# Kernel tuning notes

Hardware: AMD Instinct MI355X
Metric: run time of the kernel (lower is better)

## Reference

```python
import jax, jax.numpy as jnp
import numpy as np

B, Q, D, H, W_OUT = 1024, 128, 64, 256, 32
PI = float(np.pi)
LN_EPS = 1e-5


def setup_inputs() -> dict:
    key = jax.random.key(0)
    ks = jax.random.split(key, 18)

    def u(k, shape, fan_in):
        s = 1.0 / np.sqrt(fan_in)
        return jax.random.uniform(k, shape, jnp.float32, -s, s)

    return {
        "x_in": jax.random.normal(ks[0], (B, Q, D), jnp.float32),
        "w_out": W_OUT,
        # fc_feat: Linear(3D -> H)
        "Wf": u(ks[1], (H, 3 * D), 3 * D), "bf": u(ks[2], (H,), 3 * D),
        # GRUCell(H, H): torch layout W_ih[3H,H], W_hh[3H,H]
        "W_ih": u(ks[3], (3 * H, H), H), "W_hh": u(ks[4], (3 * H, H), H),
        "b_ih": u(ks[5], (3 * H,), H), "b_hh": u(ks[6], (3 * H,), H),
        # LayerNorm(H)
        "ln_g": jnp.ones((H,), jnp.float32), "ln_b": jnp.zeros((H,), jnp.float32),
        # fc_gain: Linear(H -> D)
        "Wg": u(ks[7], (D, H), H), "bg": u(ks[8], (D,), H),
        # fc_rp: Linear(H -> 2)
        "Wrp": u(ks[9], (2, H), H), "brp": u(ks[10], (2,), H),
        # roll_gru: GRUCell(H+D, H)
        "W_ih_r": u(ks[11], (3 * H, H + D), H), "W_hh_r": u(ks[12], (3 * H, H), H),
        "b_ih_r": u(ks[13], (3 * H,), H), "b_hh_r": u(ks[14], (3 * H,), H),
        # fc_rp_r: Linear(H -> 2)
        "Wrpr": u(ks[15], (2, H), H), "brpr": u(ks[16], (2,), H),
    }


def _gru_cell(x, h, W_ih, W_hh, b_ih, b_hh):
    gi = x @ W_ih.T + b_ih      # [B,3H]
    gh = h @ W_hh.T + b_hh      # [B,3H]
    i_r, i_z, i_n = jnp.split(gi, 3, axis=-1)
    h_r, h_z, h_n = jnp.split(gh, 3, axis=-1)
    r = jax.nn.sigmoid(i_r + h_r)
    z = jax.nn.sigmoid(i_z + h_z)
    n = jnp.tanh(i_n + r * h_n)
    return (1.0 - z) * n + z * h


def _layernorm(x, g, b):
    mu = jnp.mean(x, axis=-1, keepdims=True)
    var = jnp.mean(jnp.square(x - mu), axis=-1, keepdims=True)
    return (x - mu) * jax.lax.rsqrt(var + LN_EPS) * g + b


def _rotate(x, rho, phi):
    M = x.shape[-1] // 2
    re, im = x[:, :M], x[:, M:]
    c, s = jnp.cos(phi), jnp.sin(phi)
    return jnp.concatenate([rho * (c * re - s * im), rho * (s * re + c * im)], axis=1)


def _forward(x_in, w_out, Wf, bf, W_ih, W_hh, b_ih, b_hh, ln_g, ln_b,
             Wg, bg, Wrp, brp, W_ih_r, W_hh_r, b_ih_r, b_hh_r, Wrpr, brpr):
    Bsz, q, Dd = x_in.shape
    y0 = x_in[:, 0, :]
    h0 = jnp.zeros((Bsz, W_ih.shape[1]), x_in.dtype)
    upd0 = jnp.zeros((Bsz, Dd), x_in.dtype)

    def enc_step(carry, y_t):
        x_post, h, y_prev, prev_upd = carry
        feat = jnp.concatenate([y_t - y_prev, y_t - x_post, prev_upd], axis=1)
        zf = jnp.tanh(feat @ Wf.T + bf)
        h = _layernorm(_gru_cell(zf, h, W_ih, W_hh, b_ih, b_hh), ln_g, ln_b)
        rp = h @ Wrp.T + brp
        rho = jax.nn.sigmoid(rp[:, 0:1]) * 1.25
        phi = PI * jnp.tanh(rp[:, 1:2])
        x_pri = _rotate(x_post, rho, phi)
        K = jax.nn.sigmoid(h @ Wg.T + bg)
        x_post_new = x_pri + K * (y_t - x_pri)
        return (x_post_new, h, y_t, x_post_new - x_pri), None

    ys = jnp.swapaxes(x_in, 0, 1)  # [q,B,D]
    (x_post, h, _, _), _ = jax.lax.scan(enc_step, (y0, h0, y0, upd0), ys)

    def roll_step(carry, _):
        h_r, curr = carry
        h_r = _layernorm(_gru_cell(jnp.concatenate([h_r, curr], axis=1), h_r,
                                   W_ih_r, W_hh_r, b_ih_r, b_hh_r), ln_g, ln_b)
        rp = h_r @ Wrpr.T + brpr
        rho = jax.nn.sigmoid(rp[:, 0:1]) * 1.25
        phi = PI * jnp.tanh(rp[:, 1:2])
        curr = _rotate(curr, rho, phi)
        return (h_r, curr), curr

    _, preds = jax.lax.scan(roll_step, (h, x_post), None, length=w_out)  # [w_out,B,D]
    return jnp.swapaxes(preds, 0, 1)  # [B,w_out,D]


def reference(x_in, w_out, Wf, bf, W_ih, W_hh, b_ih, b_hh, ln_g, ln_b,
              Wg, bg, Wrp, brp, W_ih_r, W_hh_r, b_ih_r, b_hh_r, Wrpr, brpr):
    return _forward(x_in, w_out, Wf, bf, W_ih, W_hh, b_ih, b_hh, ln_g, ln_b,
                    Wg, bg, Wrp, brp, W_ih_r, W_hh_r, b_ih_r, b_hh_r, Wrpr, brpr)
```

## Files before the change

kernel.cpp:

```cpp
#include <hip/hip_runtime.h>

#define QLEN 128
#define WOUT 32
#define ROWS 4
#define PI_F 3.14159265358979f

typedef __attribute__((ext_vector_type(2))) float f32x2;

#define OFF_BF    0
#define OFF_BIH   256
#define OFF_BHH   1024
#define OFF_LNG   1792
#define OFF_LNB   2048
#define OFF_BG    2304
#define OFF_BRP   2368
#define OFF_BIHR  2370
#define OFF_BHHR  3138
#define OFF_BRPR  3906
#define OFF_WRP   3908
#define OFF_WRPR  4420
#define SB_TOTAL  4932

__device__ __forceinline__ float sigm(float x){ return 1.0f/(1.0f + __expf(-x)); }
__device__ __forceinline__ float tanh_f(float x){ return 2.0f/(1.0f + __expf(-2.0f*x)) - 1.0f; }

__device__ __forceinline__ void barrier_lgkm(){
  asm volatile("s_waitcnt lgkmcnt(0)" ::: "memory");
  __builtin_amdgcn_s_barrier();
  asm volatile("" ::: "memory");
}

__device__ __forceinline__ void pkfma(f32x2& acc, f32x2 a, f32x2 b){
  asm("v_pk_fma_f32 %0, %1, %2, %0" : "+v"(acc) : "v"(a), "v"(b));
}
__device__ __forceinline__ void fma4p(f32x2& acc, const float4& a, const float4& w){
  f32x2 alo = {a.x, a.y}, ahi = {a.z, a.w};
  f32x2 wlo = {w.x, w.y}, whi = {w.z, w.w};
  pkfma(acc, alo, wlo); pkfma(acc, ahi, whi);
}
__device__ __forceinline__ float hadd(f32x2 v){ return v[0] + v[1]; }

__global__ void transpose_w(const float* __restrict__ src, float* __restrict__ dst, int N, int K){
  int i = blockIdx.x*blockDim.x + threadIdx.x;
  if (i < N*K){
    int c = i / K; int k = i - c*K;
    dst[(size_t)(((k>>2)*N + c)<<2) + (k&3)] = src[i];
  }
}

__global__ __launch_bounds__(1024) void knet_v9(
  const float* __restrict__ x_in,
  const float* __restrict__ t_wf,
  const float* __restrict__ t_wih,
  const float* __restrict__ t_whh,
  const float* __restrict__ t_wg,
  const float* __restrict__ t_wihr,
  const float* __restrict__ t_whhr,
  const float* __restrict__ p_bf,  const float* __restrict__ p_bih, const float* __restrict__ p_bhh,
  const float* __restrict__ p_lng, const float* __restrict__ p_lnb,
  const float* __restrict__ p_bg,  const float* __restrict__ p_wrp, const float* __restrict__ p_brp,
  const float* __restrict__ p_bihr,const float* __restrict__ p_bhhr,
  const float* __restrict__ p_wrpr,const float* __restrict__ p_brpr,
  float* __restrict__ out)
{
  __shared__ __align__(16) float sb[SB_TOTAL];
  __shared__ __align__(16) float s_h  [ROWS][260];
  __shared__ __align__(16) float s_pre[ROWS][260];
  __shared__ __align__(16) float s_zf [ROWS][260];
  __shared__ __align__(16) float s_feat[ROWS][196];
  __shared__ __align__(16) float s_x  [ROWS][64];
  __shared__ __align__(16) float s_part[4][6][ROWS][256];
  __shared__ float s_rho[ROWS], s_phi[ROWS];

  const int tid = threadIdx.x;
  const int gb0 = blockIdx.x * ROWS;

  if (tid<256){ sb[OFF_BF+tid]=p_bf[tid]; sb[OFF_LNG+tid]=p_lng[tid]; sb[OFF_LNB+tid]=p_lnb[tid]; }
  if (tid<768){ sb[OFF_BIH+tid]=p_bih[tid]; sb[OFF_BHH+tid]=p_bhh[tid]; sb[OFF_BIHR+tid]=p_bihr[tid]; sb[OFF_BHHR+tid]=p_bhhr[tid]; }
  if (tid<64)  sb[OFF_BG+tid]=p_bg[tid];
  if (tid<512){ sb[OFF_WRP+tid]=p_wrp[tid]; sb[OFF_WRPR+tid]=p_wrpr[tid]; }
  if (tid<2){ sb[OFF_BRP+tid]=p_brp[tid]; sb[OFF_BRPR+tid]=p_brpr[tid]; }
  for (int e=tid; e<ROWS*256; e+=1024){ s_h[e>>8][e&255]=0.f; }

  const int w    = tid >> 6;
  const int lane = tid & 63;
  const int g4   = tid >> 8;
  const int j256 = tid & 255;
  const int j6   = tid & 63;

  const int pr = tid >> 6;
  const int pd = tid & 63;
  float y_cur = 0.f, x_st = 0.f;
  if (tid < 256){
    y_cur = x_in[(size_t)(gb0+pr)*(QLEN*64) + pd];
    x_st  = y_cur;
    s_x[pr][pd] = x_st;
    s_feat[pr][pd] = 0.f; s_feat[pr][64+pd] = 0.f; s_feat[pr][128+pd] = 0.f;
  }

  const float4* tf  = (const float4*)t_wf;
  const float4* tih = (const float4*)t_wih;
  const float4* thh = (const float4*)t_whh;
  const float4* tg  = (const float4*)t_wg;
  const float4* tir = (const float4*)t_wihr;
  const float4* th2 = (const float4*)t_whhr;
  const int k0B = g4*12;
  const int k0C = g4*16;

  __syncthreads();

  auto ln_rp = [&](int wrpO, int brpO){
    if (w < ROWS){
      const int row = w;
      const int c0  = lane << 2;
      float4 v = *(const float4*)&s_pre[row][c0];
      float sum = v.x+v.y+v.z+v.w;
      float ss  = v.x*v.x + v.y*v.y + v.z*v.z + v.w*v.w;
      #pragma unroll
      for (int m=1;m<64;m<<=1){ sum += __shfl_xor(sum,m); ss += __shfl_xor(ss,m); }
      float mu = sum * (1.f/256.f);
      float rs = rsqrtf(ss*(1.f/256.f) - mu*mu + 1e-5f);
      float4 hn;
      hn.x = (v.x-mu)*rs*sb[OFF_LNG+c0  ] + sb[OFF_LNB+c0  ];
      hn.y = (v.y-mu)*rs*sb[OFF_LNG+c0+1] + sb[OFF_LNB+c0+1];
      hn.z = (v.z-mu)*rs*sb[OFF_LNG+c0+2] + sb[OFF_LNB+c0+2];
      hn.w = (v.w-mu)*rs*sb[OFF_LNG+c0+3] + sb[OFF_LNB+c0+3];
      *(float4*)&s_h[row][c0] = hn;
      float p0 = hn.x*sb[wrpO+c0] + hn.y*sb[wrpO+c0+1] + hn.z*sb[wrpO+c0+2] + hn.w*sb[wrpO+c0+3];
      float p1 = hn.x*sb[wrpO+256+c0] + hn.y*sb[wrpO+256+c0+1] + hn.z*sb[wrpO+256+c0+2] + hn.w*sb[wrpO+256+c0+3];
      #pragma unroll
      for (int m=1;m<64;m<<=1){ p0 += __shfl_xor(p0,m); p1 += __shfl_xor(p1,m); }
      if (lane==0){
        s_rho[row] = 1.25f * sigm(p0 + sb[brpO]);
        s_phi[row] = PI_F * tanh_f(p1 + sb[brpO+1]);
      }
    }
  };

  #pragma unroll 1
  for (int t=0; t<QLEN; ++t){
    float y_next = 0.f;
    if (tid < 256){
      const int tn = (t+1<QLEN)? t+1 : QLEN-1;
      y_next = x_in[(size_t)(gb0+pr)*(QLEN*64) + (size_t)tn*64 + pd];
    }

    {
      f32x2 a0={0.f,0.f},a1={0.f,0.f},a2={0.f,0.f},a3={0.f,0.f};
      #pragma unroll 4
      for (int k4=k0B;k4<k0B+12;k4++){
        float4 wv = tf[k4*256 + j256];
        float4 f0=*(const float4*)&s_feat[0][k4<<2];
        float4 f1=*(const float4*)&s_feat[1][k4<<2];
        float4 f2=*(const float4*)&s_feat[2][k4<<2];
        float4 f3=*(const float4*)&s_feat[3][k4<<2];
        fma4p(a0,f0,wv); fma4p(a1,f1,wv); fma4p(a2,f2,wv); fma4p(a3,f3,wv);
      }
      s_part[g4][0][0][j256]=hadd(a0); s_part[g4][0][1][j256]=hadd(a1);
      s_part[g4][0][2][j256]=hadd(a2); s_part[g4][0][3][j256]=hadd(a3);
    }
    {
      f32x2 a[3][ROWS];
      #pragma unroll
      for (int gg=0;gg<3;gg++)
        #pragma unroll
        for (int ri=0;ri<ROWS;ri++) a[gg][ri]=(f32x2){0.f,0.f};
      #pragma unroll 2
      for (int k4=k0C;k4<k0C+16;k4++){
        const int base=k4*768 + j256;
        float4 whr=thh[base], whz=thh[base+256], whn=thh[base+512];
        #pragma unroll
        for (int ri=0;ri<ROWS;ri++){
          float4 ah=*(const float4*)&s_h[ri][k4<<2];
          fma4p(a[0][ri],ah,whr); fma4p(a[1][ri],ah,whz); fma4p(a[2][ri],ah,whn);
        }
      }
      #pragma unroll
      for (int gg=0;gg<3;gg++)
        #pragma unroll
        for (int ri=0;ri<ROWS;ri++)
          s_part[g4][3+gg][ri][j256]=hadd(a[gg][ri]);
    }
    barrier_lgkm();

    {
      const int r=tid>>8, jj=tid&255;
      s_zf[r][jj] = tanh_f(s_part[0][0][r][jj]+s_part[1][0][r][jj]
                          +s_part[2][0][r][jj]+s_part[3][0][r][jj] + sb[OFF_BF+jj]);
    }
    barrier_lgkm();

    {
      f32x2 a[3][ROWS];
      #pragma unroll
      for (int gg=0;gg<3;gg++)
        #pragma unroll
        for (int ri=0;ri<ROWS;ri++) a[gg][ri]=(f32x2){0.f,0.f};
      #pragma unroll 4
      for (int k4=k0C;k4<k0C+16;k4++){
        const int base=k4*768 + j256;
        float4 wir=tih[base], wiz=tih[base+256], win=tih[base+512];
        #pragma unroll
        for (int ri=0;ri<ROWS;ri++){
          float4 az=*(const float4*)&s_zf[ri][k4<<2];
          fma4p(a[0][ri],az,wir); fma4p(a[1][ri],az,wiz); fma4p(a[2][ri],az,win);
        }
      }
      #pragma unroll
      for (int gg=0;gg<3;gg++)
        #pragma unroll
        for (int ri=0;ri<ROWS;ri++)
          s_part[g4][gg][ri][j256]=hadd(a[gg][ri]);
    }
    barrier_lgkm();

    {
      const int r=tid>>8, jj=tid&255;
      float s0=s_part[0][0][r][jj]+s_part[1][0][r][jj]+s_part[2][0][r][jj]+s_part[3][0][r][jj];
      float s1=s_part[0][1][r][jj]+s_part[1][1][r][jj]+s_part[2][1][r][jj]+s_part[3][1][r][jj];
      float s2=s_part[0][2][r][jj]+s_part[1][2][r][jj]+s_part[2][2][r][jj]+s_part[3][2][r][jj];
      float s3=s_part[0][3][r][jj]+s_part[1][3][r][jj]+s_part[2][3][r][jj]+s_part[3][3][r][jj];
      float s4=s_part[0][4][r][jj]+s_part[1][4][r][jj]+s_part[2][4][r][jj]+s_part[3][4][r][jj];
      float s5=s_part[0][5][r][jj]+s_part[1][5][r][jj]+s_part[2][5][r][jj]+s_part[3][5][r][jj];
      float r_ = sigm(s0+sb[OFF_BIH+jj]     + s3+sb[OFF_BHH+jj]);
      float z_ = sigm(s1+sb[OFF_BIH+256+jj] + s4+sb[OFF_BHH+256+jj]);
      float n_ = tanh_f(s2+sb[OFF_BIH+512+jj] + r_*(s5+sb[OFF_BHH+512+jj]));
      s_pre[r][jj] = (1.f - z_)*n_ + z_*s_h[r][jj];
    }
    barrier_lgkm();

    ln_rp(OFF_WRP, OFF_BRP);
    barrier_lgkm();

    {
      f32x2 acc[ROWS];
      #pragma unroll
      for (int ri=0;ri<ROWS;ri++) acc[ri]=(f32x2){0.f,0.f};
      const int kb = w*4;
      #pragma unroll
      for (int q=0;q<4;q++){
        float4 wv = tg[(kb+q)*64 + j6];
        #pragma unroll
        for (int ri=0;ri<ROWS;ri++){
          float4 ah=*(const float4*)&s_h[ri][(kb+q)<<2];
          fma4p(acc[ri],ah,wv);
        }
      }
      #pragma unroll
      for (int ri=0;ri<ROWS;ri++) s_part[w>>2][0][ri][(w&3)*64 + j6] = hadd(acc[ri]);
    }
    barrier_lgkm();

    if (tid < 256){
      float kacc = sb[OFF_BG+pd];
      #pragma unroll
      for (int q=0;q<16;q++) kacc += s_part[q>>2][0][pr][(q&3)*64+pd];
      float kg = sigm(kacc);
      float rho=s_rho[pr], phi=s_phi[pr];
      float sn,cs; __sincosf(phi,&sn,&cs);
      float px = __shfl_xor(x_st,32);
      float pre = (pd<32) ? rho*(cs*x_st - sn*px) : rho*(sn*px + cs*x_st);
      float del = kg*(y_cur - pre);
      x_st = pre + del;
      s_x[pr][pd] = x_st;
      s_feat[pr][pd]      = y_next - y_cur;
      s_feat[pr][64+pd]   = y_next - x_st;
      s_feat[pr][128+pd]  = del;
      y_cur = y_next;
    }
    barrier_lgkm();
  }

  #pragma unroll 1
  for (int u=0; u<WOUT; ++u){
    {
      f32x2 a[6][ROWS];
      #pragma unroll
      for (int gg=0;gg<6;gg++)
        #pragma unroll
        for (int ri=0;ri<ROWS;ri++) a[gg][ri]=(f32x2){0.f,0.f};
      if (g4 < 3){
        const int k0i=g4*20;
        #pragma unroll 2
        for (int k4=k0i;k4<k0i+20;k4++){
          const int base=k4*768 + j256;
          float4 wir=tir[base], wiz=tir[base+256], win=tir[base+512];
          #pragma unroll
          for (int ri=0;ri<ROWS;ri++){
            float4 ah=*(const float4*)&s_h[ri][k4<<2];
            fma4p(a[0][ri],ah,wir); fma4p(a[1][ri],ah,wiz); fma4p(a[2][ri],ah,win);
          }
        }
      } else {
        #pragma unroll
        for (int k4=60;k4<64;k4++){
          const int base=k4*768 + j256;
          float4 wir=tir[base], wiz=tir[base+256], win=tir[base+512];
          #pragma unroll
          for (int ri=0;ri<ROWS;ri++){
            float4 ah=*(const float4*)&s_h[ri][k4<<2];
            fma4p(a[0][ri],ah,wir); fma4p(a[1][ri],ah,wiz); fma4p(a[2][ri],ah,win);
          }
        }
        #pragma unroll 2
        for (int k4=64;k4<80;k4++){
          const int base=k4*768 + j256;
          float4 wir=tir[base], wiz=tir[base+256], win=tir[base+512];
          #pragma unroll
          for (int ri=0;ri<ROWS;ri++){
            float4 ax=*(const float4*)&s_x[ri][(k4-64)<<2];
            fma4p(a[0][ri],ax,wir); fma4p(a[1][ri],ax,wiz); fma4p(a[2][ri],ax,win);
          }
        }
      }
      {
        #pragma unroll 2
        for (int k4=k0C;k4<k0C+16;k4++){
          const int base=k4*768 + j256;
          float4 whr=th2[base], whz=th2[base+256], whn=th2[base+512];
          #pragma unroll
          for (int ri=0;ri<ROWS;ri++){
            float4 ah=*(const float4*)&s_h[ri][k4<<2];
            fma4p(a[3][ri],ah,whr); fma4p(a[4][ri],ah,whz); fma4p(a[5][ri],ah,whn);
          }
        }
      }
      #pragma unroll
      for (int gg=0;gg<6;gg++)
        #pragma unroll
        for (int ri=0;ri<ROWS;ri++)
          s_part[g4][gg][ri][j256]=hadd(a[gg][ri]);
    }
    barrier_lgkm();

    {
      const int r=tid>>8, jj=tid&255;
      float s0=s_part[0][0][r][jj]+s_part[1][0][r][jj]+s_part[2][0][r][jj]+s_part[3][0][r][jj];
      float s1=s_part[0][1][r][jj]+s_part[1][1][r][jj]+s_part[2][1][r][jj]+s_part[3][1][r][jj];
      float s2=s_part[0][2][r][jj]+s_part[1][2][r][jj]+s_part[2][2][r][jj]+s_part[3][2][r][jj];
      float s3=s_part[0][3][r][jj]+s_part[1][3][r][jj]+s_part[2][3][r][jj]+s_part[3][3][r][jj];
      float s4=s_part[0][4][r][jj]+s_part[1][4][r][jj]+s_part[2][4][r][jj]+s_part[3][4][r][jj];
      float s5=s_part[0][5][r][jj]+s_part[1][5][r][jj]+s_part[2][5][r][jj]+s_part[3][5][r][jj];
      float r_ = sigm(s0+sb[OFF_BIHR+jj]     + s3+sb[OFF_BHHR+jj]);
      float z_ = sigm(s1+sb[OFF_BIHR+256+jj] + s4+sb[OFF_BHHR+256+jj]);
      float n_ = tanh_f(s2+sb[OFF_BIHR+512+jj] + r_*(s5+sb[OFF_BHHR+512+jj]));
      s_pre[r][jj] = (1.f - z_)*n_ + z_*s_h[r][jj];
    }
    barrier_lgkm();

    ln_rp(OFF_WRPR, OFF_BRPR);
    barrier_lgkm();

    if (tid < 256){
      float rho=s_rho[pr], phi=s_phi[pr];
      float sn,cs; __sincosf(phi,&sn,&cs);
      float px = __shfl_xor(x_st,32);
      float nx = (pd<32) ? rho*(cs*x_st - sn*px) : rho*(sn*px + cs*x_st);
      x_st = nx;
      s_x[pr][pd] = nx;
      out[(size_t)(gb0+pr)*(WOUT*64) + (size_t)u*64 + pd] = nx;
    }
    barrier_lgkm();
  }
}

extern "C" void kernel_launch(void* const* d_in, const int* in_sizes, int n_in,
                              void* d_out, int out_size, void* d_ws, size_t ws_size,
                              hipStream_t stream){
  const float* x_in = (const float*)d_in[0];
  const float* Wf   = (const float*)d_in[2];
  const float* bf_  = (const float*)d_in[3];
  const float* Wih  = (const float*)d_in[4];
  const float* Whh  = (const float*)d_in[5];
  const float* bih  = (const float*)d_in[6];
  const float* bhh  = (const float*)d_in[7];
  const float* lng  = (const float*)d_in[8];
  const float* lnb  = (const float*)d_in[9];
  const float* Wg   = (const float*)d_in[10];
  const float* bg   = (const float*)d_in[11];
  const float* Wrp  = (const float*)d_in[12];
  const float* brp  = (const float*)d_in[13];
  const float* Wihr = (const float*)d_in[14];
  const float* Whhr = (const float*)d_in[15];
  const float* bihr = (const float*)d_in[16];
  const float* bhhr = (const float*)d_in[17];
  const float* Wrpr = (const float*)d_in[18];
  const float* brpr = (const float*)d_in[19];

  float* ws = (float*)d_ws;
  float* t_wf   = ws;
  float* t_wih  = ws + 49152;
  float* t_whh  = ws + 245760;
  float* t_wg   = ws + 442368;
  float* t_wihr = ws + 458752;
  float* t_whhr = ws + 704512;

  transpose_w<<<(49152 +255)/256, 256, 0, stream>>>(Wf,   t_wf,   256, 192);
  transpose_w<<<(196608+255)/256, 256, 0, stream>>>(Wih,  t_wih,  768, 256);
  transpose_w<<<(196608+255)/256, 256, 0, stream>>>(Whh,  t_whh,  768, 256);
  transpose_w<<<(16384 +255)/256, 256, 0, stream>>>(Wg,   t_wg,   64,  256);
  transpose_w<<<(245760+255)/256, 256, 0, stream>>>(Wihr, t_wihr, 768, 320);
  transpose_w<<<(196608+255)/256, 256, 0, stream>>>(Whhr, t_whhr, 768, 256);

  knet_v9<<<256, 1024, 0, stream>>>(x_in, t_wf, t_wih, t_whh, t_wg, t_wihr, t_whhr,
      bf_, bih, bhh, lng, lnb, bg, Wrp, brp, bihr, bhhr, Wrpr, brpr,
      (float*)d_out);
}
```

Baseline: 2.986 ms.

## Fold LayerNorm into gain matmul and prefetch first weight tiles across barriers

Precomputes Wg scaled by the LayerNorm gain together with per-output constants, so the Kalman gain is computed from the pre-norm hidden state with a mean/rstd correction. This lets waves 4-5 run the gain matmul concurrently with the LN/rp wave, which removes one barrier per encoder step. It also prefetches the first k-slice of the Wf, Whh, Wih and Wih_r weights before barriers to hide global-load latency, at the cost of extra live registers. Folding the LayerNorm changes rounding slightly.

```diff
diff --git a/kernel.cpp b/kernel.cpp
--- a/kernel.cpp
+++ b/kernel.cpp
@@ -19,7 +19,9 @@
 #define OFF_BRPR  3906
 #define OFF_WRP   3908
 #define OFF_WRPR  4420
-#define SB_TOTAL  4932
+#define OFF_C1    4932
+#define OFF_C2    4996
+#define SB_TOTAL  5060
 
 __device__ __forceinline__ float sigm(float x){ return 1.0f/(1.0f + __expf(-x)); }
 __device__ __forceinline__ float tanh_f(float x){ return 2.0f/(1.0f + __expf(-2.0f*x)) - 1.0f; }
@@ -48,17 +50,35 @@
   }
 }
 
-__global__ __launch_bounds__(1024) void knet_v9(
+__global__ void prep_wg(const float* __restrict__ Wg, const float* __restrict__ lng,
+                        const float* __restrict__ lnb, const float* __restrict__ bg,
+                        float* __restrict__ wg2, float* __restrict__ c1, float* __restrict__ c2){
+  int j = threadIdx.x;
+  if (j < 64){
+    float a1=0.f, a2=0.f;
+    for (int k=0;k<256;k++){
+      float wv = Wg[j*256+k];
+      float gw = lng[k]*wv;
+      wg2[(size_t)(((k>>2)*64 + j)<<2) + (k&3)] = gw;
+      a1 += gw;
+      a2 += lnb[k]*wv;
+    }
+    c1[j]=a1; c2[j]=a2+bg[j];
+  }
+}
+
+__global__ __launch_bounds__(1024) void knet_v10(
   const float* __restrict__ x_in,
   const float* __restrict__ t_wf,
   const float* __restrict__ t_wih,
   const float* __restrict__ t_whh,
-  const float* __restrict__ t_wg,
+  const float* __restrict__ wg2p,
   const float* __restrict__ t_wihr,
   const float* __restrict__ t_whhr,
+  const float* __restrict__ c1p, const float* __restrict__ c2p,
   const float* __restrict__ p_bf,  const float* __restrict__ p_bih, const float* __restrict__ p_bhh,
   const float* __restrict__ p_lng, const float* __restrict__ p_lnb,
-  const float* __restrict__ p_bg,  const float* __restrict__ p_wrp, const float* __restrict__ p_brp,
+  const float* __restrict__ p_wrp, const float* __restrict__ p_brp,
   const float* __restrict__ p_bihr,const float* __restrict__ p_bhhr,
   const float* __restrict__ p_wrpr,const float* __restrict__ p_brpr,
   float* __restrict__ out)
@@ -70,14 +90,14 @@
   __shared__ __align__(16) float s_feat[ROWS][196];
   __shared__ __align__(16) float s_x  [ROWS][64];
   __shared__ __align__(16) float s_part[4][6][ROWS][256];
-  __shared__ float s_rho[ROWS], s_phi[ROWS];
+  __shared__ float s_rho[ROWS], s_phi[ROWS], s_mu[ROWS], s_rs[ROWS];
 
   const int tid = threadIdx.x;
   const int gb0 = blockIdx.x * ROWS;
 
   if (tid<256){ sb[OFF_BF+tid]=p_bf[tid]; sb[OFF_LNG+tid]=p_lng[tid]; sb[OFF_LNB+tid]=p_lnb[tid]; }
   if (tid<768){ sb[OFF_BIH+tid]=p_bih[tid]; sb[OFF_BHH+tid]=p_bhh[tid]; sb[OFF_BIHR+tid]=p_bihr[tid]; sb[OFF_BHHR+tid]=p_bhhr[tid]; }
-  if (tid<64)  sb[OFF_BG+tid]=p_bg[tid];
+  if (tid<64){ sb[OFF_C1+tid]=c1p[tid]; sb[OFF_C2+tid]=c2p[tid]; }
   if (tid<512){ sb[OFF_WRP+tid]=p_wrp[tid]; sb[OFF_WRPR+tid]=p_wrpr[tid]; }
   if (tid<2){ sb[OFF_BRP+tid]=p_brp[tid]; sb[OFF_BRPR+tid]=p_brpr[tid]; }
   for (int e=tid; e<ROWS*256; e+=1024){ s_h[e>>8][e&255]=0.f; }
@@ -86,7 +106,6 @@
   const int lane = tid & 63;
   const int g4   = tid >> 8;
   const int j256 = tid & 255;
-  const int j6   = tid & 63;
 
   const int pr = tid >> 6;
   const int pd = tid & 63;
@@ -101,7 +120,7 @@
   const float4* tf  = (const float4*)t_wf;
   const float4* tih = (const float4*)t_wih;
   const float4* thh = (const float4*)t_whh;
-  const float4* tg  = (const float4*)t_wg;
+  const float4* tg2 = (const float4*)wg2p;
   const float4* tir = (const float4*)t_wihr;
   const float4* th2 = (const float4*)t_whhr;
   const int k0B = g4*12;
@@ -133,9 +152,16 @@
       if (lane==0){
         s_rho[row] = 1.25f * sigm(p0 + sb[brpO]);
         s_phi[row] = PI_F * tanh_f(p1 + sb[brpO+1]);
+        s_mu[row] = mu; s_rs[row] = rs;
       }
     }
   };
+
+  float4 pfA, pfB0, pfB1, pfB2;
+  pfA  = tf [(size_t)k0B*256 + j256];
+  pfB0 = thh[(size_t)k0C*768 + j256];
+  pfB1 = thh[(size_t)k0C*768 + 256 + j256];
+  pfB2 = thh[(size_t)k0C*768 + 512 + j256];
 
   #pragma unroll 1
   for (int t=0; t<QLEN; ++t){
@@ -147,8 +173,15 @@
 
     {
       f32x2 a0={0.f,0.f},a1={0.f,0.f},a2={0.f,0.f},a3={0.f,0.f};
+      {
+        float4 f0=*(const float4*)&s_feat[0][k0B<<2];
+        float4 f1=*(const float4*)&s_feat[1][k0B<<2];
+        float4 f2=*(const float4*)&s_feat[2][k0B<<2];
+        float4 f3=*(const float4*)&s_feat[3][k0B<<2];
+        fma4p(a0,f0,pfA); fma4p(a1,f1,pfA); fma4p(a2,f2,pfA); fma4p(a3,f3,pfA);
+      }
       #pragma unroll 4
-      for (int k4=k0B;k4<k0B+12;k4++){
+      for (int k4=k0B+1;k4<k0B+12;k4++){
         float4 wv = tf[k4*256 + j256];
         float4 f0=*(const float4*)&s_feat[0][k4<<2];
         float4 f1=*(const float4*)&s_feat[1][k4<<2];
@@ -165,8 +198,13 @@
       for (int gg=0;gg<3;gg++)
         #pragma unroll
         for (int ri=0;ri<ROWS;ri++) a[gg][ri]=(f32x2){0.f,0.f};
-      #pragma unroll 2
-      for (int k4=k0C;k4<k0C+16;k4++){
+      #pragma unroll
+      for (int ri=0;ri<ROWS;ri++){
+        float4 ah=*(const float4*)&s_h[ri][k0C<<2];
+        fma4p(a[0][ri],ah,pfB0); fma4p(a[1][ri],ah,pfB1); fma4p(a[2][ri],ah,pfB2);
+      }
+      #pragma unroll 4
+      for (int k4=k0C+1;k4<k0C+16;k4++){
         const int base=k4*768 + j256;
         float4 whr=thh[base], whz=thh[base+256], whn=thh[base+512];
         #pragma unroll
@@ -183,6 +221,9 @@
     }
     barrier_lgkm();
 
+    float4 pz0 = tih[(size_t)k0C*768 + j256];
+    float4 pz1 = tih[(size_t)k0C*768 + 256 + j256];
+    float4 pz2 = tih[(size_t)k0C*768 + 512 + j256];
     {
       const int r=tid>>8, jj=tid&255;
       s_zf[r][jj] = tanh_f(s_part[0][0][r][jj]+s_part[1][0][r][jj]
@@ -196,8 +237,13 @@
       for (int gg=0;gg<3;gg++)
         #pragma unroll
         for (int ri=0;ri<ROWS;ri++) a[gg][ri]=(f32x2){0.f,0.f};
+      #pragma unroll
+      for (int ri=0;ri<ROWS;ri++){
+        float4 az=*(const float4*)&s_zf[ri][k0C<<2];
+        fma4p(a[0][ri],az,pz0); fma4p(a[1][ri],az,pz1); fma4p(a[2][ri],az,pz2);
+      }
       #pragma unroll 4
-      for (int k4=k0C;k4<k0C+16;k4++){
+      for (int k4=k0C+1;k4<k0C+16;k4++){
         const int base=k4*768 + j256;
         float4 wir=tih[base], wiz=tih[base+256], win=tih[base+512];
         #pragma unroll
@@ -230,32 +276,32 @@
     barrier_lgkm();
 
     ln_rp(OFF_WRP, OFF_BRP);
-    barrier_lgkm();
-
-    {
+    if (w==4 || w==5){
+      const int eg = w-4, ej = lane;
       f32x2 acc[ROWS];
       #pragma unroll
       for (int ri=0;ri<ROWS;ri++) acc[ri]=(f32x2){0.f,0.f};
-      const int kb = w*4;
-      #pragma unroll
-      for (int q=0;q<4;q++){
-        float4 wv = tg[(kb+q)*64 + j6];
+      #pragma unroll 4
+      for (int k4=eg*32; k4<eg*32+32; k4++){
+        float4 wv = tg2[k4*64 + ej];
         #pragma unroll
         for (int ri=0;ri<ROWS;ri++){
-          float4 ah=*(const float4*)&s_h[ri][(kb+q)<<2];
-          fma4p(acc[ri],ah,wv);
-        }
-      }
-      #pragma unroll
-      for (int ri=0;ri<ROWS;ri++) s_part[w>>2][0][ri][(w&3)*64 + j6] = hadd(acc[ri]);
-    }
-    barrier_lgkm();
-
+          float4 ap=*(const float4*)&s_pre[ri][k4<<2];
+          fma4p(acc[ri],ap,wv);
+        }
+      }
+      #pragma unroll
+      for (int ri=0;ri<ROWS;ri++) s_part[eg][0][ri][ej] = hadd(acc[ri]);
+    }
+    barrier_lgkm();
+
+    pfA  = tf [(size_t)k0B*256 + j256];
+    pfB0 = thh[(size_t)k0C*768 + j256];
+    pfB1 = thh[(size_t)k0C*768 + 256 + j256];
+    pfB2 = thh[(size_t)k0C*768 + 512 + j256];
     if (tid < 256){
-      float kacc = sb[OFF_BG+pd];
-      #pragma unroll
-      for (int q=0;q<16;q++) kacc += s_part[q>>2][0][pr][(q&3)*64+pd];
-      float kg = sigm(kacc);
+      float S1 = s_part[0][0][pr][pd] + s_part[1][0][pr][pd];
+      float kg = sigm( s_rs[pr]*(S1 - s_mu[pr]*sb[OFF_C1+pd]) + sb[OFF_C2+pd] );
       float rho=s_rho[pr], phi=s_phi[pr];
       float sn,cs; __sincosf(phi,&sn,&cs);
       float px = __shfl_xor(x_st,32);
@@ -271,6 +317,11 @@
     barrier_lgkm();
   }
 
+  const int k0i = (g4<3)? g4*20 : 60;
+  float4 pi0 = tir[(size_t)k0i*768 + j256];
+  float4 pi1 = tir[(size_t)k0i*768 + 256 + j256];
+  float4 pi2 = tir[(size_t)k0i*768 + 512 + j256];
+
   #pragma unroll 1
   for (int u=0; u<WOUT; ++u){
     {
@@ -279,10 +330,14 @@
       for (int gg=0;gg<6;gg++)
         #pragma unroll
         for (int ri=0;ri<ROWS;ri++) a[gg][ri]=(f32x2){0.f,0.f};
+      #pragma unroll
+      for (int ri=0;ri<ROWS;ri++){
+        float4 ah=*(const float4*)&s_h[ri][k0i<<2];
+        fma4p(a[0][ri],ah,pi0); fma4p(a[1][ri],ah,pi1); fma4p(a[2][ri],ah,pi2);
+      }
       if (g4 < 3){
-        const int k0i=g4*20;
         #pragma unroll 2
-        for (int k4=k0i;k4<k0i+20;k4++){
+        for (int k4=k0i+1;k4<k0i+20;k4++){
           const int base=k4*768 + j256;
           float4 wir=tir[base], wiz=tir[base+256], win=tir[base+512];
           #pragma unroll
@@ -293,7 +348,7 @@
         }
       } else {
         #pragma unroll
-        for (int k4=60;k4<64;k4++){
+        for (int k4=61;k4<64;k4++){
           const int base=k4*768 + j256;
           float4 wir=tir[base], wiz=tir[base+256], win=tir[base+512];
           #pragma unroll
@@ -351,6 +406,9 @@
     ln_rp(OFF_WRPR, OFF_BRPR);
     barrier_lgkm();
 
+    pi0 = tir[(size_t)k0i*768 + j256];
+    pi1 = tir[(size_t)k0i*768 + 256 + j256];
+    pi2 = tir[(size_t)k0i*768 + 512 + j256];
     if (tid < 256){
       float rho=s_rho[pr], phi=s_phi[pr];
       float sn,cs; __sincosf(phi,&sn,&cs);
@@ -391,18 +449,20 @@
   float* t_wf   = ws;
   float* t_wih  = ws + 49152;
   float* t_whh  = ws + 245760;
-  float* t_wg   = ws + 442368;
+  float* wg2    = ws + 442368;
   float* t_wihr = ws + 458752;
   float* t_whhr = ws + 704512;
+  float* c1     = ws + 901120;
+  float* c2     = ws + 901184;
 
   transpose_w<<<(49152 +255)/256, 256, 0, stream>>>(Wf,   t_wf,   256, 192);
   transpose_w<<<(196608+255)/256, 256, 0, stream>>>(Wih,  t_wih,  768, 256);
   transpose_w<<<(196608+255)/256, 256, 0, stream>>>(Whh,  t_whh,  768, 256);
-  transpose_w<<<(16384 +255)/256, 256, 0, stream>>>(Wg,   t_wg,   64,  256);
   transpose_w<<<(245760+255)/256, 256, 0, stream>>>(Wihr, t_wihr, 768, 320);
   transpose_w<<<(196608+255)/256, 256, 0, stream>>>(Whhr, t_whhr, 768, 256);
-
-  knet_v9<<<256, 1024, 0, stream>>>(x_in, t_wf, t_wih, t_whh, t_wg, t_wihr, t_whhr,
-      bf_, bih, bhh, lng, lnb, bg, Wrp, brp, bihr, bhhr, Wrpr, brpr,
+  prep_wg<<<1, 64, 0, stream>>>(Wg, lng, lnb, bg, wg2, c1, c2);
+
+  knet_v10<<<256, 1024, 0, stream>>>(x_in, t_wf, t_wih, t_whh, wg2, t_wihr, t_whhr,
+      c1, c2, bf_, bih, bhh, lng, lnb, Wrp, brp, bihr, bhhr, Wrpr, brpr,
       (float*)d_out);
 }
```

After: 11.05 ms. +270.2%, slower.

## Process eight batch rows per block with 512 threads and two-way K split

Applied to the files above, without the earlier changes.

Doubles rows per block from 4 to 8 and halves threads to 512, so each weight load from global/L2 is reused across twice as many batch rows. The K dimension is now split two ways instead of four, which halves the partial-sum reduction work. Only 128 blocks launch, fewer than the CU count, so parallelism drops and each thread does twice the FMA work per step.

```diff
diff --git a/kernel.cpp b/kernel.cpp
--- a/kernel.cpp
+++ b/kernel.cpp
@@ -2,7 +2,7 @@
 
 #define QLEN 128
 #define WOUT 32
-#define ROWS 4
+#define ROWS 8
 #define PI_F 3.14159265358979f
 
 typedef __attribute__((ext_vector_type(2))) float f32x2;
@@ -48,7 +48,7 @@
   }
 }
 
-__global__ __launch_bounds__(1024) void knet_v9(
+__global__ __launch_bounds__(512, 2) void knet_v13(
   const float* __restrict__ x_in,
   const float* __restrict__ t_wf,
   const float* __restrict__ t_wih,
@@ -69,29 +69,29 @@
   __shared__ __align__(16) float s_zf [ROWS][260];
   __shared__ __align__(16) float s_feat[ROWS][196];
   __shared__ __align__(16) float s_x  [ROWS][64];
-  __shared__ __align__(16) float s_part[4][6][ROWS][256];
+  __shared__ __align__(16) float s_part[2][6][ROWS][256];
   __shared__ float s_rho[ROWS], s_phi[ROWS];
 
   const int tid = threadIdx.x;
   const int gb0 = blockIdx.x * ROWS;
 
-  if (tid<256){ sb[OFF_BF+tid]=p_bf[tid]; sb[OFF_LNG+tid]=p_lng[tid]; sb[OFF_LNB+tid]=p_lnb[tid]; }
-  if (tid<768){ sb[OFF_BIH+tid]=p_bih[tid]; sb[OFF_BHH+tid]=p_bhh[tid]; sb[OFF_BIHR+tid]=p_bihr[tid]; sb[OFF_BHHR+tid]=p_bhhr[tid]; }
-  if (tid<64)  sb[OFF_BG+tid]=p_bg[tid];
-  if (tid<512){ sb[OFF_WRP+tid]=p_wrp[tid]; sb[OFF_WRPR+tid]=p_wrpr[tid]; }
+  for (int i=tid;i<256;i+=512){ sb[OFF_BF+i]=p_bf[i]; sb[OFF_LNG+i]=p_lng[i]; sb[OFF_LNB+i]=p_lnb[i]; }
+  for (int i=tid;i<768;i+=512){ sb[OFF_BIH+i]=p_bih[i]; sb[OFF_BHH+i]=p_bhh[i]; sb[OFF_BIHR+i]=p_bihr[i]; sb[OFF_BHHR+i]=p_bhhr[i]; }
+  for (int i=tid;i<64;i+=512)  sb[OFF_BG+i]=p_bg[i];
+  for (int i=tid;i<512;i+=512){ sb[OFF_WRP+i]=p_wrp[i]; sb[OFF_WRPR+i]=p_wrpr[i]; }
   if (tid<2){ sb[OFF_BRP+tid]=p_brp[tid]; sb[OFF_BRPR+tid]=p_brpr[tid]; }
-  for (int e=tid; e<ROWS*256; e+=1024){ s_h[e>>8][e&255]=0.f; }
+  for (int e=tid; e<ROWS*256; e+=512){ s_h[e>>8][e&255]=0.f; }
 
   const int w    = tid >> 6;
   const int lane = tid & 63;
-  const int g4   = tid >> 8;
+  const int g2   = tid >> 8;
   const int j256 = tid & 255;
   const int j6   = tid & 63;
 
   const int pr = tid >> 6;
   const int pd = tid & 63;
-  float y_cur = 0.f, x_st = 0.f;
-  if (tid < 256){
+  float y_cur, x_st;
+  {
     y_cur = x_in[(size_t)(gb0+pr)*(QLEN*64) + pd];
     x_st  = y_cur;
     s_x[pr][pd] = x_st;
@@ -104,60 +104,60 @@
   const float4* tg  = (const float4*)t_wg;
   const float4* tir = (const float4*)t_wihr;
   const float4* th2 = (const float4*)t_whhr;
-  const int k0B = g4*12;
-  const int k0C = g4*16;
+  const int k0B = g2*24;
+  const int k0C = g2*32;
 
   __syncthreads();
 
   auto ln_rp = [&](int wrpO, int brpO){
-    if (w < ROWS){
-      const int row = w;
-      const int c0  = lane << 2;
-      float4 v = *(const float4*)&s_pre[row][c0];
-      float sum = v.x+v.y+v.z+v.w;
-      float ss  = v.x*v.x + v.y*v.y + v.z*v.z + v.w*v.w;
-      #pragma unroll
-      for (int m=1;m<64;m<<=1){ sum += __shfl_xor(sum,m); ss += __shfl_xor(ss,m); }
-      float mu = sum * (1.f/256.f);
-      float rs = rsqrtf(ss*(1.f/256.f) - mu*mu + 1e-5f);
-      float4 hn;
-      hn.x = (v.x-mu)*rs*sb[OFF_LNG+c0  ] + sb[OFF_LNB+c0  ];
-      hn.y = (v.y-mu)*rs*sb[OFF_LNG+c0+1] + sb[OFF_LNB+c0+1];
-      hn.z = (v.z-mu)*rs*sb[OFF_LNG+c0+2] + sb[OFF_LNB+c0+2];
-      hn.w = (v.w-mu)*rs*sb[OFF_LNG+c0+3] + sb[OFF_LNB+c0+3];
-      *(float4*)&s_h[row][c0] = hn;
-      float p0 = hn.x*sb[wrpO+c0] + hn.y*sb[wrpO+c0+1] + hn.z*sb[wrpO+c0+2] + hn.w*sb[wrpO+c0+3];
-      float p1 = hn.x*sb[wrpO+256+c0] + hn.y*sb[wrpO+256+c0+1] + hn.z*sb[wrpO+256+c0+2] + hn.w*sb[wrpO+256+c0+3];
-      #pragma unroll
-      for (int m=1;m<64;m<<=1){ p0 += __shfl_xor(p0,m); p1 += __shfl_xor(p1,m); }
-      if (lane==0){
-        s_rho[row] = 1.25f * sigm(p0 + sb[brpO]);
-        s_phi[row] = PI_F * tanh_f(p1 + sb[brpO+1]);
-      }
+    const int row = w;
+    const int c0  = lane << 2;
+    float4 v = *(const float4*)&s_pre[row][c0];
+    float sum = v.x+v.y+v.z+v.w;
+    float ss  = v.x*v.x + v.y*v.y + v.z*v.z + v.w*v.w;
+    #pragma unroll
+    for (int m=1;m<64;m<<=1){ sum += __shfl_xor(sum,m); ss += __shfl_xor(ss,m); }
+    float mu = sum * (1.f/256.f);
+    float rs = rsqrtf(ss*(1.f/256.f) - mu*mu + 1e-5f);
+    float4 hn;
+    hn.x = (v.x-mu)*rs*sb[OFF_LNG+c0  ] + sb[OFF_LNB+c0  ];
+    hn.y = (v.y-mu)*rs*sb[OFF_LNG+c0+1] + sb[OFF_LNB+c0+1];
+    hn.z = (v.z-mu)*rs*sb[OFF_LNG+c0+2] + sb[OFF_LNB+c0+2];
+    hn.w = (v.w-mu)*rs*sb[OFF_LNG+c0+3] + sb[OFF_LNB+c0+3];
+    *(float4*)&s_h[row][c0] = hn;
+    float p0 = hn.x*sb[wrpO+c0] + hn.y*sb[wrpO+c0+1] + hn.z*sb[wrpO+c0+2] + hn.w*sb[wrpO+c0+3];
+    float p1 = hn.x*sb[wrpO+256+c0] + hn.y*sb[wrpO+256+c0+1] + hn.z*sb[wrpO+256+c0+2] + hn.w*sb[wrpO+256+c0+3];
+    #pragma unroll
+    for (int m=1;m<64;m<<=1){ p0 += __shfl_xor(p0,m); p1 += __shfl_xor(p1,m); }
+    if (lane==0){
+      s_rho[row] = 1.25f * sigm(p0 + sb[brpO]);
+      s_phi[row] = PI_F * tanh_f(p1 + sb[brpO+1]);
     }
   };
 
   #pragma unroll 1
   for (int t=0; t<QLEN; ++t){
-    float y_next = 0.f;
-    if (tid < 256){
+    float y_next;
+    {
       const int tn = (t+1<QLEN)? t+1 : QLEN-1;
       y_next = x_in[(size_t)(gb0+pr)*(QLEN*64) + (size_t)tn*64 + pd];
     }
 
     {
-      f32x2 a0={0.f,0.f},a1={0.f,0.f},a2={0.f,0.f},a3={0.f,0.f};
+      f32x2 a[ROWS];
+      #pragma unroll
+      for (int ri=0;ri<ROWS;ri++) a[ri]=(f32x2){0.f,0.f};
       #pragma unroll 4
-      for (int k4=k0B;k4<k0B+12;k4++){
+      for (int k4=k0B;k4<k0B+24;k4++){
         float4 wv = tf[k4*256 + j256];
-        float4 f0=*(const float4*)&s_feat[0][k4<<2];
-        float4 f1=*(const float4*)&s_feat[1][k4<<2];
-        float4 f2=*(const float4*)&s_feat[2][k4<<2];
-        float4 f3=*(const float4*)&s_feat[3][k4<<2];
-        fma4p(a0,f0,wv); fma4p(a1,f1,wv); fma4p(a2,f2,wv); fma4p(a3,f3,wv);
-      }
-      s_part[g4][0][0][j256]=hadd(a0); s_part[g4][0][1][j256]=hadd(a1);
-      s_part[g4][0][2][j256]=hadd(a2); s_part[g4][0][3][j256]=hadd(a3);
+        #pragma unroll
+        for (int ri=0;ri<ROWS;ri++){
+          float4 f=*(const float4*)&s_feat[ri][k4<<2];
+          fma4p(a[ri],f,wv);
+        }
+      }
+      #pragma unroll
+      for (int ri=0;ri<ROWS;ri++) s_part[g2][0][ri][j256]=hadd(a[ri]);
     }
     {
       f32x2 a[3][ROWS];
@@ -166,7 +166,7 @@
         #pragma unroll
         for (int ri=0;ri<ROWS;ri++) a[gg][ri]=(f32x2){0.f,0.f};
       #pragma unroll 2
-      for (int k4=k0C;k4<k0C+16;k4++){
+      for (int k4=k0C;k4<k0C+32;k4++){
         const int base=k4*768 + j256;
         float4 whr=thh[base], whz=thh[base+256], whn=thh[base+512];
         #pragma unroll
@@ -179,14 +179,13 @@
       for (int gg=0;gg<3;gg++)
         #pragma unroll
         for (int ri=0;ri<ROWS;ri++)
-          s_part[g4][3+gg][ri][j256]=hadd(a[gg][ri]);
-    }
-    barrier_lgkm();
-
-    {
-      const int r=tid>>8, jj=tid&255;
-      s_zf[r][jj] = tanh_f(s_part[0][0][r][jj]+s_part[1][0][r][jj]
-                          +s_part[2][0][r][jj]+s_part[3][0][r][jj] + sb[OFF_BF+jj]);
+          s_part[g2][3+gg][ri][j256]=hadd(a[gg][ri]);
+    }
+    barrier_lgkm();
+
+    for (int e=tid; e<ROWS*256; e+=512){
+      const int r=e>>8, jj=e&255;
+      s_zf[r][jj] = tanh_f(s_part[0][0][r][jj]+s_part[1][0][r][jj] + sb[OFF_BF+jj]);
     }
     barrier_lgkm();
 
@@ -196,8 +195,8 @@
       for (int gg=0;gg<3;gg++)
         #pragma unroll
         for (int ri=0;ri<ROWS;ri++) a[gg][ri]=(f32x2){0.f,0.f};
-      #pragma unroll 4
-      for (int k4=k0C;k4<k0C+16;k4++){
+      #pragma unroll 2
+      for (int k4=k0C;k4<k0C+32;k4++){
         const int base=k4*768 + j256;
         float4 wir=tih[base], wiz=tih[base+256], win=tih[base+512];
         #pragma unroll
@@ -210,18 +209,18 @@
       for (int gg=0;gg<3;gg++)
         #pragma unroll
         for (int ri=0;ri<ROWS;ri++)
-          s_part[g4][gg][ri][j256]=hadd(a[gg][ri]);
-    }
-    barrier_lgkm();
-
-    {
-      const int r=tid>>8, jj=tid&255;
-      float s0=s_part[0][0][r][jj]+s_part[1][0][r][jj]+s_part[2][0][r][jj]+s_part[3][0][r][jj];
-      float s1=s_part[0][1][r][jj]+s_part[1][1][r][jj]+s_part[2][1][r][jj]+s_part[3][1][r][jj];
-      float s2=s_part[0][2][r][jj]+s_part[1][2][r][jj]+s_part[2][2][r][jj]+s_part[3][2][r][jj];
-      float s3=s_part[0][3][r][jj]+s_part[1][3][r][jj]+s_part[2][3][r][jj]+s_part[3][3][r][jj];
-      float s4=s_part[0][4][r][jj]+s_part[1][4][r][jj]+s_part[2][4][r][jj]+s_part[3][4][r][jj];
-      float s5=s_part[0][5][r][jj]+s_part[1][5][r][jj]+s_part[2][5][r][jj]+s_part[3][5][r][jj];
+          s_part[g2][gg][ri][j256]=hadd(a[gg][ri]);
+    }
+    barrier_lgkm();
+
+    for (int e=tid; e<ROWS*256; e+=512){
+      const int r=e>>8, jj=e&255;
+      float s0=s_part[0][0][r][jj]+s_part[1][0][r][jj];
+      float s1=s_part[0][1][r][jj]+s_part[1][1][r][jj];
+      float s2=s_part[0][2][r][jj]+s_part[1][2][r][jj];
+      float s3=s_part[0][3][r][jj]+s_part[1][3][r][jj];
+      float s4=s_part[0][4][r][jj]+s_part[1][4][r][jj];
+      float s5=s_part[0][5][r][jj]+s_part[1][5][r][jj];
       float r_ = sigm(s0+sb[OFF_BIH+jj]     + s3+sb[OFF_BHH+jj]);
       float z_ = sigm(s1+sb[OFF_BIH+256+jj] + s4+sb[OFF_BHH+256+jj]);
       float n_ = tanh_f(s2+sb[OFF_BIH+512+jj] + r_*(s5+sb[OFF_BHH+512+jj]));
@@ -236,9 +235,9 @@
       f32x2 acc[ROWS];
       #pragma unroll
       for (int ri=0;ri<ROWS;ri++) acc[ri]=(f32x2){0.f,0.f};
-      const int kb = w*4;
-      #pragma unroll
-      for (int q=0;q<4;q++){
+      const int kb = w*8;
+      #pragma unroll
+      for (int q=0;q<8;q++){
         float4 wv = tg[(kb+q)*64 + j6];
         #pragma unroll
         for (int ri=0;ri<ROWS;ri++){
@@ -247,14 +246,14 @@
         }
       }
       #pragma unroll
-      for (int ri=0;ri<ROWS;ri++) s_part[w>>2][0][ri][(w&3)*64 + j6] = hadd(acc[ri]);
-    }
-    barrier_lgkm();
-
-    if (tid < 256){
+      for (int ri=0;ri<ROWS;ri++) s_part[w&1][0][ri][(w>>1)*64 + j6] = hadd(acc[ri]);
+    }
+    barrier_lgkm();
+
+    {
       float kacc = sb[OFF_BG+pd];
       #pragma unroll
-      for (int q=0;q<16;q++) kacc += s_part[q>>2][0][pr][(q&3)*64+pd];
+      for (int q=0;q<8;q++) kacc += s_part[q&1][0][pr][(q>>1)*64+pd];
       float kg = sigm(kacc);
       float rho=s_rho[pr], phi=s_phi[pr];
       float sn,cs; __sincosf(phi,&sn,&cs);
@@ -279,10 +278,9 @@
       for (int gg=0;gg<6;gg++)
         #pragma unroll
         for (int ri=0;ri<ROWS;ri++) a[gg][ri]=(f32x2){0.f,0.f};
-      if (g4 < 3){
-        const int k0i=g4*20;
+      if (g2 == 0){
         #pragma unroll 2
-        for (int k4=k0i;k4<k0i+20;k4++){
+        for (int k4=0;k4<40;k4++){
           const int base=k4*768 + j256;
           float4 wir=tir[base], wiz=tir[base+256], win=tir[base+512];
           #pragma unroll
@@ -292,8 +290,8 @@
           }
         }
       } else {
-        #pragma unroll
-        for (int k4=60;k4<64;k4++){
+        #pragma unroll 2
+        for (int k4=40;k4<64;k4++){
           const int base=k4*768 + j256;
           float4 wir=tir[base], wiz=tir[base+256], win=tir[base+512];
           #pragma unroll
@@ -315,7 +313,7 @@
       }
       {
         #pragma unroll 2
-        for (int k4=k0C;k4<k0C+16;k4++){
+        for (int k4=k0C;k4<k0C+32;k4++){
           const int base=k4*768 + j256;
           float4 whr=th2[base], whz=th2[base+256], whn=th2[base+512];
           #pragma unroll
@@ -329,18 +327,18 @@
       for (int gg=0;gg<6;gg++)
         #pragma unroll
         for (int ri=0;ri<ROWS;ri++)
-          s_part[g4][gg][ri][j256]=hadd(a[gg][ri]);
-    }
-    barrier_lgkm();
-
-    {
-      const int r=tid>>8, jj=tid&255;
-      float s0=s_part[0][0][r][jj]+s_part[1][0][r][jj]+s_part[2][0][r][jj]+s_part[3][0][r][jj];
-      float s1=s_part[0][1][r][jj]+s_part[1][1][r][jj]+s_part[2][1][r][jj]+s_part[3][1][r][jj];
-      float s2=s_part[0][2][r][jj]+s_part[1][2][r][jj]+s_part[2][2][r][jj]+s_part[3][2][r][jj];
-      float s3=s_part[0][3][r][jj]+s_part[1][3][r][jj]+s_part[2][3][r][jj]+s_part[3][3][r][jj];
-      float s4=s_part[0][4][r][jj]+s_part[1][4][r][jj]+s_part[2][4][r][jj]+s_part[3][4][r][jj];
-      float s5=s_part[0][5][r][jj]+s_part[1][5][r][jj]+s_part[2][5][r][jj]+s_part[3][5][r][jj];
+          s_part[g2][gg][ri][j256]=hadd(a[gg][ri]);
+    }
+    barrier_lgkm();
+
+    for (int e=tid; e<ROWS*256; e+=512){
+      const int r=e>>8, jj=e&255;
+      float s0=s_part[0][0][r][jj]+s_part[1][0][r][jj];
+      float s1=s_part[0][1][r][jj]+s_part[1][1][r][jj];
+      float s2=s_part[0][2][r][jj]+s_part[1][2][r][jj];
+      float s3=s_part[0][3][r][jj]+s_part[1][3][r][jj];
+      float s4=s_part[0][4][r][jj]+s_part[1][4][r][jj];
+      float s5=s_part[0][5][r][jj]+s_part[1][5][r][jj];
       float r_ = sigm(s0+sb[OFF_BIHR+jj]     + s3+sb[OFF_BHHR+jj]);
       float z_ = sigm(s1+sb[OFF_BIHR+256+jj] + s4+sb[OFF_BHHR+256+jj]);
       float n_ = tanh_f(s2+sb[OFF_BIHR+512+jj] + r_*(s5+sb[OFF_BHHR+512+jj]));
@@ -351,7 +349,7 @@
     ln_rp(OFF_WRPR, OFF_BRPR);
     barrier_lgkm();
 
-    if (tid < 256){
+    {
       float rho=s_rho[pr], phi=s_phi[pr];
       float sn,cs; __sincosf(phi,&sn,&cs);
       float px = __shfl_xor(x_st,32);
@@ -402,7 +400,7 @@
   transpose_w<<<(245760+255)/256, 256, 0, stream>>>(Wihr, t_wihr, 768, 320);
   transpose_w<<<(196608+255)/256, 256, 0, stream>>>(Whhr, t_whhr, 768, 256);
 
-  knet_v9<<<256, 1024, 0, stream>>>(x_in, t_wf, t_wih, t_whh, t_wg, t_wihr, t_whhr,
+  knet_v13<<<128, 512, 0, stream>>>(x_in, t_wf, t_wih, t_whh, t_wg, t_wihr, t_whhr,
       bf_, bih, bhh, lng, lnb, bg, Wrp, brp, bihr, bhhr, Wrpr, brpr,
       (float*)d_out);
 }
```

New measurement: 3.996 ms. +33.8%, slower.
